# Performance work log

Hardware: AMD Instinct MI355X
Metric: run time of the kernel (lower is better)

The kernel has to match this reference:

```python
import jax, jax.numpy as jnp
import numpy as np

N = 50000      # nodes
NE = 512000    # edges
D = 128        # in_dim = out_dim
H = 8          # heads
DH = D // H    # 16, head dim
EPS_BN = 1e-5


def _bn(x, g, b):
    # training-mode BatchNorm1d: biased batch stats
    m = x.mean(0)
    v = x.var(0)
    return g * (x - m) / jnp.sqrt(v + EPS_BN) + b


def setup_inputs() -> dict:
    key = jax.random.key(0)
    ks = jax.random.split(key, 16)
    s = 0.02
    return {
        "h": jax.random.normal(ks[0], (N, D), jnp.float32),
        "e": jax.random.normal(ks[1], (NE, D), jnp.float32),
        "src": jax.random.randint(ks[2], (NE,), 0, N, jnp.int32),
        "dst": jax.random.randint(ks[3], (NE,), 0, N, jnp.int32),
        "Wq": jax.random.normal(ks[4], (D, D), jnp.float32) * s,
        "Wk": jax.random.normal(ks[5], (D, D), jnp.float32) * s,
        "Wv": jax.random.normal(ks[6], (D, D), jnp.float32) * s,
        "We": jax.random.normal(ks[7], (D, D), jnp.float32) * s,
        "Wo": jax.random.normal(ks[8], (D, D), jnp.float32) * s,
        "bo": jnp.zeros((D,), jnp.float32),
        "g1h": jnp.ones((D,), jnp.float32), "b1h": jnp.zeros((D,), jnp.float32),
        "g1e": jnp.ones((D,), jnp.float32), "b1e": jnp.zeros((D,), jnp.float32),
        "W1": jax.random.normal(ks[9], (D, 2 * D), jnp.float32) * s,
        "b1": jnp.zeros((2 * D,), jnp.float32),
        "W2": jax.random.normal(ks[10], (2 * D, D), jnp.float32) * s,
        "b2": jnp.zeros((D,), jnp.float32),
        "g2h": jnp.ones((D,), jnp.float32), "b2h": jnp.zeros((D,), jnp.float32),
    }


def reference(h, e, src, dst, Wq, Wk, Wv, We, Wo, bo,
              g1h, b1h, g1e, b1e, W1, b1, W2, b2, g2h, b2h):
    # --- multi-head edge attention ---
    Q = (h @ Wq).reshape(N, H, DH)
    K = (h @ Wk).reshape(N, H, DH)
    V = (h @ Wv).reshape(N, H, DH)
    Eh = (e @ We).reshape(NE, H, DH)
    # per-edge score: K[src]*Q[dst] / sqrt(DH), times edge features, exp-clamped
    score = (K[src] * Q[dst]) / np.sqrt(DH) * Eh            # [NE,H,DH]
    s = jnp.exp(jnp.clip(score.sum(-1), -5.0, 5.0))          # [NE,H]
    # scatter-sum to destination nodes
    wV = jax.ops.segment_sum(V[src] * s[:, :, None], dst, num_segments=N)  # [N,H,DH]
    z = jax.ops.segment_sum(s, dst, num_segments=N)                         # [N,H]
    h_attn = wV / (z[:, :, None] + 1e-6)

    # --- output proj + residual + batch norm ---
    h2 = h_attn.reshape(N, D) @ Wo + bo
    h2 = h + h2
    e2 = e + Eh.reshape(NE, D)
    h2 = _bn(h2, g1h, b1h)
    e2 = _bn(e2, g1e, b1e)

    # --- FFN + residual + batch norm ---
    r = jax.nn.relu(h2 @ W1 + b1) @ W2 + b2
    h3 = _bn(h2 + r, g2h, b2h)
    return h3, e2
```

## Files before the change

### kernel.cpp

```cpp
#include <hip/hip_runtime.h>
#include <math.h>

#define NN 50000
#define NEDGE 512000
#define DD 128

typedef short bf16x8 __attribute__((ext_vector_type(8)));
typedef float f32x4 __attribute__((ext_vector_type(4)));

__device__ __forceinline__ short f2bf(float f){
  union { float f; unsigned u; } v; v.f = f;
  unsigned u = v.u;
  return (short)((u + 0x7fffu + ((u >> 16) & 1u)) >> 16);
}
__device__ __forceinline__ float bf2f(short s){
  union { unsigned u; float f; } v; v.u = ((unsigned)(unsigned short)s) << 16; return v.f;
}

__device__ __forceinline__ bf16x8 packA(const float* __restrict__ rowp, int kbase){
  float4 x = *(const float4*)(rowp + kbase);
  float4 y = *(const float4*)(rowp + kbase + 4);
  bf16x8 r;
  r[0]=f2bf(x.x); r[1]=f2bf(x.y); r[2]=f2bf(x.z); r[3]=f2bf(x.w);
  r[4]=f2bf(y.x); r[5]=f2bf(y.y); r[6]=f2bf(y.z); r[7]=f2bf(y.w);
  return r;
}

__global__ __launch_bounds__(256) void prep_hist(
    const float* __restrict__ Wq, const float* __restrict__ Wk,
    const float* __restrict__ Wv, const float* __restrict__ We,
    const float* __restrict__ Wo, const float* __restrict__ W1,
    const float* __restrict__ W2, short* __restrict__ wdst,
    const int* __restrict__ dst, int* __restrict__ counts){
  if (blockIdx.x >= 576){
    int id = (blockIdx.x-576)*256 + threadIdx.x;
    if (id < NEDGE) atomicAdd(&counts[dst[id]], 1);
    return;
  }
  int id = blockIdx.x*256 + threadIdx.x;
  const float* src; short* dstp; int K, NCOL, local;
  if (id < 81920){
    int m = id >> 14; local = id & 16383; K = 128; NCOL = 128;
    src = (m==0)?Wq:(m==1)?Wk:(m==2)?Wv:(m==3)?We:Wo;
    dstp = wdst + m*16384;
  } else if (id < 114688){
    local = id - 81920; K = 128; NCOL = 256; src = W1; dstp = wdst + 81920;
  } else if (id < 147456){
    local = id - 114688; K = 256; NCOL = 128; src = W2; dstp = wdst + 114688;
  } else return;
  int k = local / NCOL, n = local % NCOL;
  dstp[n*K + k] = f2bf(src[local]);
}

#define SCAN_NB 196
__global__ __launch_bounds__(256) void scan_p1(
    const int* __restrict__ counts, int* __restrict__ bsum){
  int idx = blockIdx.x*256 + threadIdx.x;
  int v = (idx < NN) ? counts[idx] : 0;
  __shared__ int sd[256];
  sd[threadIdx.x] = v; __syncthreads();
  for (int o=128;o>0;o>>=1){
    if (threadIdx.x < o) sd[threadIdx.x] += sd[threadIdx.x+o];
    __syncthreads();
  }
  if (threadIdx.x == 0) bsum[blockIdx.x] = sd[0];
}
__global__ __launch_bounds__(256) void scan_p2(
    const int* __restrict__ bsum, int* __restrict__ bbase){
  int t = threadIdx.x;
  int v = (t < SCAN_NB) ? bsum[t] : 0;
  __shared__ int ps[256];
  ps[t] = v; __syncthreads();
  for (int o=1;o<256;o<<=1){
    int x = (t>=o) ? ps[t-o] : 0;
    __syncthreads();
    ps[t] += x;
    __syncthreads();
  }
  if (t < SCAN_NB) bbase[t] = ps[t] - v;
}
__global__ __launch_bounds__(256) void scan_p3(
    const int* __restrict__ counts, const int* __restrict__ bbase,
    int* __restrict__ off){
  int t = threadIdx.x;
  int idx = blockIdx.x*256 + t;
  int v = (idx < NN) ? counts[idx] : 0;
  __shared__ int ps[256];
  ps[t] = v; __syncthreads();
  for (int o=1;o<256;o<<=1){
    int x = (t>=o) ? ps[t-o] : 0;
    __syncthreads();
    ps[t] += x;
    __syncthreads();
  }
  if (idx < NN) off[idx] = bbase[blockIdx.x] + ps[t] - v;
  if (blockIdx.x == 0 && t == 0) off[NN] = NEDGE;
}

__global__ __launch_bounds__(256) void qkv_scatter(
    const float* __restrict__ h, const short* __restrict__ wT,
    short* __restrict__ QbP, short* __restrict__ KbP, short* __restrict__ Vb,
    const int* __restrict__ dst, const int* __restrict__ off,
    int* __restrict__ cursor, int* __restrict__ perm){
  if (blockIdx.x >= 782){
    int id = (blockIdx.x-782)*256 + threadIdx.x;
    if (id < NEDGE){
      int d = dst[id];
      int r = atomicAdd(&cursor[d], 1);
      perm[off[d] + r] = id;
    }
    return;
  }
  const short* WqT = wT;
  const short* WkT = wT + 16384;
  const short* WvT = wT + 32768;
  int lane = threadIdx.x & 63, wave = threadIdx.x >> 6;
  int r16 = lane & 15, kg = lane >> 4;
  int rowbase = blockIdx.x*64 + wave*16;
  int arow = rowbase + r16; if (arow > NN-1) arow = NN-1;
  const float* Arow = h + (size_t)arow*DD;
  f32x4 acc[3][8];
  #pragma unroll
  for (int m=0;m<3;m++)
    #pragma unroll
    for (int j=0;j<8;j++) acc[m][j] = (f32x4){0.f,0.f,0.f,0.f};
  #pragma unroll
  for (int kc=0;kc<4;kc++){
    int kb = kc*32 + kg*8;
    bf16x8 a = packA(Arow, kb);
    #pragma unroll
    for (int j=0;j<8;j++){
      bf16x8 bq = *(const bf16x8*)(WqT + (j*16+r16)*DD + kb);
      acc[0][j] = __builtin_amdgcn_mfma_f32_16x16x32_bf16(a, bq, acc[0][j], 0,0,0);
      bf16x8 bk = *(const bf16x8*)(WkT + (j*16+r16)*DD + kb);
      acc[1][j] = __builtin_amdgcn_mfma_f32_16x16x32_bf16(a, bk, acc[1][j], 0,0,0);
      bf16x8 bv = *(const bf16x8*)(WvT + (j*16+r16)*DD + kb);
      acc[2][j] = __builtin_amdgcn_mfma_f32_16x16x32_bf16(a, bv, acc[2][j], 0,0,0);
    }
  }
  int orow0 = rowbase + kg*4;
  #pragma unroll
  for (int j=0;j<8;j++){
    #pragma unroll
    for (int r=0;r<4;r++){
      int row = orow0 + r;
      if (row < NN){
        QbP[(size_t)row*DD + r16*8 + j] = f2bf(acc[0][j][r]);
        KbP[(size_t)row*DD + r16*8 + j] = f2bf(acc[1][j][r]);
        Vb [(size_t)row*DD + j*16 + r16] = f2bf(acc[2][j][r]);
      }
    }
  }
}

__global__ __launch_bounds__(256) void edge_fused(
    const float* __restrict__ e, const short* __restrict__ WeT,
    const short* __restrict__ QbP, const short* __restrict__ KbP,
    const int* __restrict__ src, const int* __restrict__ dst,
    short* __restrict__ e2p, short* __restrict__ sArrB,
    short* __restrict__ partB){
  __shared__ short eL[64*128];
  int tid = threadIdx.x;
  int rowbase = blockIdx.x*64;
  int lane = tid & 63, wave = tid >> 6;
  int c = lane & 15, kg = lane >> 4;
  bf16x8 kv[4], qv[4];
  #pragma unroll
  for (int r=0;r<4;r++){
    int ed = rowbase + wave*16 + kg*4 + r;
    int sj = src[ed], dj = dst[ed];
    kv[r] = *(const bf16x8*)(KbP + (size_t)sj*DD + c*8);
    qv[r] = *(const bf16x8*)(QbP + (size_t)dj*DD + c*8);
  }
  {
    int row = wave*16 + (lane >> 2);
    int c0  = (lane & 3) * 32;
    const float* rp = e + (size_t)(rowbase+row)*DD + c0;
    #pragma unroll
    for (int g=0; g<4; ++g){
      float4 x = *(const float4*)(rp + g*8);
      float4 y = *(const float4*)(rp + g*8 + 4);
      bf16x8 v;
      v[0]=f2bf(x.x); v[1]=f2bf(x.y); v[2]=f2bf(x.z); v[3]=f2bf(x.w);
      v[4]=f2bf(y.x); v[5]=f2bf(y.y); v[6]=f2bf(y.z); v[7]=f2bf(y.w);
      int col8 = (c0 >> 3) + g;
      *(bf16x8*)&eL[row*DD + ((col8 ^ (row&7))<<3)] = v;
    }
  }
  f32x4 acc[8];
  #pragma unroll
  for (int j=0;j<8;j++) acc[j] = (f32x4){0.f,0.f,0.f,0.f};
  int arow = wave*16 + c;
  #pragma unroll
  for (int kc=0;kc<4;kc++){
    int col8 = kc*4 + kg;
    bf16x8 a = *(const bf16x8*)&eL[arow*DD + ((col8 ^ (arow&7))<<3)];
    int kb = kc*32 + kg*8;
    #pragma unroll
    for (int j=0;j<8;j++){
      bf16x8 b = *(const bf16x8*)(WeT + (j*16+c)*DD + kb);
      acc[j] = __builtin_amdgcn_mfma_f32_16x16x32_bf16(a, b, acc[j], 0,0,0);
    }
  }
  float ssum[8], ssq[8];
  #pragma unroll
  for (int j=0;j<8;j++){ ssum[j]=0.f; ssq[j]=0.f; }
  #pragma unroll
  for (int r=0;r<4;r++){
    int le = wave*16 + kg*4 + r;
    int sw = le & 7;
    int rowoff = le*DD;
    #pragma unroll
    for (int j=0;j<8;j++){
      int col = j*16 + c;
      int sidx = rowoff + (((col>>3) ^ sw)<<3) + (col & 7);
      float v = bf2f(eL[sidx]) + acc[j][r];
      eL[sidx] = f2bf(v);
      ssum[j] += v; ssq[j] += v*v;
    }
  }
  #pragma unroll
  for (int j=0;j<8;j++){
    ssum[j] += __shfl_xor(ssum[j],16); ssum[j] += __shfl_xor(ssum[j],32);
    ssq[j]  += __shfl_xor(ssq[j],16);  ssq[j]  += __shfl_xor(ssq[j],32);
  }
  if (kg == 0){
    size_t pb = ((size_t)blockIdx.x*4 + wave)*256;
    #pragma unroll
    for (int j=0;j<8;j++){
      partB[pb + j*16 + c]       = f2bf(ssum[j]);
      partB[pb + 128 + j*16 + c] = f2bf(ssq[j]);
    }
  }
  #pragma unroll
  for (int r=0;r<4;r++){
    int ed = rowbase + wave*16 + kg*4 + r;
    float sreg = 0.f;
    #pragma unroll
    for (int j=0;j<8;j++){
      float p = bf2f(kv[r][j]) * bf2f(qv[r][j]) * acc[j][r];
      p += __shfl_xor(p,1); p += __shfl_xor(p,2);
      p += __shfl_xor(p,4); p += __shfl_xor(p,8);
      if (c == j) sreg = p;
    }
    if (c < 8){
      float s = __expf(fminf(fmaxf(sreg*0.25f,-5.f),5.f));
      sArrB[(size_t)ed*8 + c] = f2bf(s);
    }
  }
  #pragma unroll
  for (int it=0; it<4; ++it){
    int row = wave*16 + it*4 + (lane>>4);
    int col8 = lane & 15;
    bf16x8 v = *(const bf16x8*)&eL[row*DD + ((col8 ^ (row&7))<<3)];
    *(bf16x8*)(e2p + (size_t)(rowbase+row)*DD + col8*8) = v;
  }
}

__global__ __launch_bounds__(256) void agg_bn(
    const int* __restrict__ off, const int* __restrict__ perm,
    const int* __restrict__ src, const short* __restrict__ sArrB,
    const short* __restrict__ Vb, short* __restrict__ hA,
    const short* __restrict__ e2p, const float* __restrict__ ssE,
    float* __restrict__ e2){
  if (blockIdx.x >= 12500){
    size_t gi0 = (size_t)(blockIdx.x-12500)*256 + threadIdx.x;
    int col0 = (int)(gi0 & 15) * 8;
    float scr[8], shr[8];
    #pragma unroll
    for (int i=0;i<8;i++){ scr[i]=ssE[col0+i]; shr[i]=ssE[DD+col0+i]; }
    size_t stride = (size_t)2048*256;
    size_t total = (size_t)NEDGE*16;
    for (size_t gi = gi0; gi < total; gi += stride){
      bf16x8 v = *(const bf16x8*)(e2p + gi*8);
      float4 o0, o1;
      o0.x = bf2f(v[0])*scr[0]+shr[0];
      o0.y = bf2f(v[1])*scr[1]+shr[1];
      o0.z = bf2f(v[2])*scr[2]+shr[2];
      o0.w = bf2f(v[3])*scr[3]+shr[3];
      o1.x = bf2f(v[4])*scr[4]+shr[4];
      o1.y = bf2f(v[5])*scr[5]+shr[5];
      o1.z = bf2f(v[6])*scr[6]+shr[6];
      o1.w = bf2f(v[7])*scr[7]+shr[7];
      *(float4*)(e2 + gi*8)     = o0;
      *(float4*)(e2 + gi*8 + 4) = o1;
    }
    return;
  }
  int wave = threadIdx.x >> 6, lane = threadIdx.x & 63;
  int node = blockIdx.x*4 + wave;
  if (node >= NN) return;
  int beg = off[node], end = off[node+1];
  int col2 = lane*2;
  int hd = lane >> 3;
  float w0 = 0.f, w1 = 0.f, zh = 0.f;
  int ed = beg;
  for (; ed+3 < end; ed += 4){
    int pe0 = perm[ed],   pe1 = perm[ed+1];
    int pe2 = perm[ed+2], pe3 = perm[ed+3];
    int sj0 = src[pe0], sj1 = src[pe1], sj2 = src[pe2], sj3 = src[pe3];
    float s0 = bf2f(sArrB[(size_t)pe0*8 + hd]);
    float s1 = bf2f(sArrB[(size_t)pe1*8 + hd]);
    float s2 = bf2f(sArrB[(size_t)pe2*8 + hd]);
    float s3 = bf2f(sArrB[(size_t)pe3*8 + hd]);
    unsigned v0 = *(const unsigned*)(Vb + (size_t)sj0*DD + col2);
    unsigned v1 = *(const unsigned*)(Vb + (size_t)sj1*DD + col2);
    unsigned v2 = *(const unsigned*)(Vb + (size_t)sj2*DD + col2);
    unsigned v3 = *(const unsigned*)(Vb + (size_t)sj3*DD + col2);
    w0 += bf2f((short)(v0 & 0xffff))*s0 + bf2f((short)(v1 & 0xffff))*s1
        + bf2f((short)(v2 & 0xffff))*s2 + bf2f((short)(v3 & 0xffff))*s3;
    w1 += bf2f((short)(v0 >> 16))*s0 + bf2f((short)(v1 >> 16))*s1
        + bf2f((short)(v2 >> 16))*s2 + bf2f((short)(v3 >> 16))*s3;
    zh += s0 + s1 + s2 + s3;
  }
  for (; ed < end; ++ed){
    int pe = perm[ed];
    int sj = src[pe];
    float s = bf2f(sArrB[(size_t)pe*8 + hd]);
    unsigned vv = *(const unsigned*)(Vb + (size_t)sj*DD + col2);
    w0 += bf2f((short)(vv & 0xffff)) * s;
    w1 += bf2f((short)(vv >> 16)) * s;
    zh += s;
  }
  float inv = 1.f/(zh + 1e-6f);
  unsigned outv = (((unsigned)(unsigned short)f2bf(w1*inv)) << 16)
                |  ((unsigned)(unsigned short)f2bf(w0*inv));
  *(unsigned*)(hA + (size_t)node*DD + col2) = outv;
}

__global__ __launch_bounds__(256) void attn_out(
    const short* __restrict__ hA,
    const short* __restrict__ WoT, const float* __restrict__ bo,
    const float* __restrict__ h, short* __restrict__ h2pre,
    float* __restrict__ part){
  int lane = threadIdx.x & 63, wave = threadIdx.x >> 6;
  int r16 = lane & 15, kg = lane >> 4;
  int rowbase = blockIdx.x*64 + wave*16;
  int arow = rowbase + r16; if (arow > NN-1) arow = NN-1;
  const short* Arow = hA + (size_t)arow*DD;
  f32x4 acc[8];
  #pragma unroll
  for (int j=0;j<8;j++) acc[j] = (f32x4){0.f,0.f,0.f,0.f};
  #pragma unroll
  for (int kc=0;kc<4;kc++){
    int kb = kc*32 + kg*8;
    bf16x8 a = *(const bf16x8*)(Arow + kb);
    #pragma unroll
    for (int j=0;j<8;j++){
      bf16x8 b = *(const bf16x8*)(WoT + (j*16+r16)*DD + kb);
      acc[j] = __builtin_amdgcn_mfma_f32_16x16x32_bf16(a, b, acc[j], 0,0,0);
    }
  }
  int orow0 = rowbase + kg*4;
  float ssum[8], ssq[8];
  #pragma unroll
  for (int j=0;j<8;j++){ ssum[j]=0.f; ssq[j]=0.f; }
  #pragma unroll
  for (int j=0;j<8;j++){
    #pragma unroll
    for (int r=0;r<4;r++){
      int row = orow0 + r;
      if (row < NN){
        int col = j*16 + r16;
        float v = acc[j][r] + bo[col] + h[(size_t)row*DD + col];
        h2pre[(size_t)row*DD + col] = f2bf(v);
        ssum[j] += v; ssq[j] += v*v;
      }
    }
  }
  #pragma unroll
  for (int j=0;j<8;j++){
    ssum[j] += __shfl_xor(ssum[j],16); ssum[j] += __shfl_xor(ssum[j],32);
    ssq[j]  += __shfl_xor(ssq[j],16);  ssq[j]  += __shfl_xor(ssq[j],32);
  }
  if (kg == 0){
    size_t pb = ((size_t)blockIdx.x*4 + wave)*256;
    #pragma unroll
    for (int j=0;j<8;j++){
      part[pb + j*16 + r16]       = ssum[j];
      part[pb + 128 + j*16 + r16] = ssq[j];
    }
  }
}

__global__ __launch_bounds__(256) void ffn1_gemm(
    const short* __restrict__ h2pre, const float* __restrict__ ss1,
    const short* __restrict__ W1T, const float* __restrict__ b1,
    short* __restrict__ ffn1){
  int lane = threadIdx.x & 63, wave = threadIdx.x >> 6;
  int r16 = lane & 15, kg = lane >> 4;
  int rowbase = blockIdx.x*64 + wave*16;
  int arow = rowbase + r16; if (arow > NN-1) arow = NN-1;
  const short* Arow = h2pre + (size_t)arow*DD;
  f32x4 acc[16];
  #pragma unroll
  for (int j=0;j<16;j++) acc[j] = (f32x4){0.f,0.f,0.f,0.f};
  #pragma unroll
  for (int kc=0;kc<4;kc++){
    int kb = kc*32 + kg*8;
    bf16x8 raw = *(const bf16x8*)(Arow + kb);
    float4 s0 = *(const float4*)(ss1 + kb);
    float4 s1 = *(const float4*)(ss1 + kb + 4);
    float4 t0 = *(const float4*)(ss1 + DD + kb);
    float4 t1 = *(const float4*)(ss1 + DD + kb + 4);
    bf16x8 a;
    a[0]=f2bf(bf2f(raw[0])*s0.x+t0.x); a[1]=f2bf(bf2f(raw[1])*s0.y+t0.y);
    a[2]=f2bf(bf2f(raw[2])*s0.z+t0.z); a[3]=f2bf(bf2f(raw[3])*s0.w+t0.w);
    a[4]=f2bf(bf2f(raw[4])*s1.x+t1.x); a[5]=f2bf(bf2f(raw[5])*s1.y+t1.y);
    a[6]=f2bf(bf2f(raw[6])*s1.z+t1.z); a[7]=f2bf(bf2f(raw[7])*s1.w+t1.w);
    #pragma unroll
    for (int j=0;j<16;j++){
      bf16x8 b = *(const bf16x8*)(W1T + (j*16+r16)*DD + kb);
      acc[j] = __builtin_amdgcn_mfma_f32_16x16x32_bf16(a, b, acc[j], 0,0,0);
    }
  }
  int orow0 = rowbase + kg*4;
  #pragma unroll
  for (int j=0;j<16;j++){
    #pragma unroll
    for (int r=0;r<4;r++){
      int row = orow0 + r;
      if (row < NN){
        int col = j*16 + r16;
        float v = fmaxf(acc[j][r] + b1[col], 0.f);
        ffn1[(size_t)row*256 + col] = f2bf(v);
      }
    }
  }
}

__global__ __launch_bounds__(256) void ffn2_gemm(
    const short* __restrict__ ffn1, const short* __restrict__ W2T,
    const float* __restrict__ b2, const short* __restrict__ h2pre,
    const float* __restrict__ ss1, float* __restrict__ h3pre,
    float* __restrict__ part){
  int lane = threadIdx.x & 63, wave = threadIdx.x >> 6;
  int r16 = lane & 15, kg = lane >> 4;
  int rowbase = blockIdx.x*64 + wave*16;
  int arow = rowbase + r16; if (arow > NN-1) arow = NN-1;
  const short* Arow = ffn1 + (size_t)arow*256;
  f32x4 acc[8];
  #pragma unroll
  for (int j=0;j<8;j++) acc[j] = (f32x4){0.f,0.f,0.f,0.f};
  #pragma unroll
  for (int kc=0;kc<8;kc++){
    int kb = kc*32 + kg*8;
    bf16x8 a = *(const bf16x8*)(Arow + kb);
    #pragma unroll
    for (int j=0;j<8;j++){
      bf16x8 b = *(const bf16x8*)(W2T + (j*16+r16)*256 + kb);
      acc[j] = __builtin_amdgcn_mfma_f32_16x16x32_bf16(a, b, acc[j], 0,0,0);
    }
  }
  int orow0 = rowbase + kg*4;
  float ssum[8], ssq[8];
  #pragma unroll
  for (int j=0;j<8;j++){ ssum[j]=0.f; ssq[j]=0.f; }
  #pragma unroll
  for (int j=0;j<8;j++){
    #pragma unroll
    for (int r=0;r<4;r++){
      int row = orow0 + r;
      if (row < NN){
        int col = j*16 + r16;
        float x = bf2f(h2pre[(size_t)row*DD + col]);
        float h2bn = x*ss1[col] + ss1[DD+col];
        float v = h2bn + acc[j][r] + b2[col];
        h3pre[(size_t)row*DD + col] = v;
        ssum[j] += v; ssq[j] += v*v;
      }
    }
  }
  #pragma unroll
  for (int j=0;j<8;j++){
    ssum[j] += __shfl_xor(ssum[j],16); ssum[j] += __shfl_xor(ssum[j],32);
    ssq[j]  += __shfl_xor(ssq[j],16);  ssq[j]  += __shfl_xor(ssq[j],32);
  }
  if (kg == 0){
    size_t pb = ((size_t)blockIdx.x*4 + wave)*256;
    #pragma unroll
    for (int j=0;j<8;j++){
      part[pb + j*16 + r16]       = ssum[j];
      part[pb + 128 + j*16 + r16] = ssq[j];
    }
  }
}

__global__ __launch_bounds__(256) void bn_reduce(
    const float* __restrict__ part, int nparts, float inv_n,
    const float* __restrict__ g, const float* __restrict__ b,
    float* __restrict__ ss){
  int col = blockIdx.x, t = threadIdx.x;
  float s = 0.f, q = 0.f;
  for (int i=t; i<nparts; i+=256){
    s += part[(size_t)i*256 + col];
    q += part[(size_t)i*256 + DD + col];
  }
  __shared__ float ls[256], lq[256];
  ls[t] = s; lq[t] = q; __syncthreads();
  for (int o2=128; o2>0; o2>>=1){
    if (t < o2){ ls[t] += ls[t+o2]; lq[t] += lq[t+o2]; }
    __syncthreads();
  }
  if (t == 0){
    float mean = ls[0]*inv_n;
    float var  = lq[0]*inv_n - mean*mean;
    float sc = g[col]*rsqrtf(var + 1e-5f);
    ss[col]      = sc;
    ss[DD + col] = b[col] - mean*sc;
  }
}

__global__ __launch_bounds__(256) void bn_reduce_bf16(
    const short* __restrict__ part, int nparts, float inv_n,
    const float* __restrict__ g, const float* __restrict__ b,
    float* __restrict__ ss){
  int col = blockIdx.x, t = threadIdx.x;
  float s = 0.f, q = 0.f;
  for (int i=t; i<nparts; i+=256){
    s += bf2f(part[(size_t)i*256 + col]);
    q += bf2f(part[(size_t)i*256 + DD + col]);
  }
  __shared__ float ls[256], lq[256];
  ls[t] = s; lq[t] = q; __syncthreads();
  for (int o2=128; o2>0; o2>>=1){
    if (t < o2){ ls[t] += ls[t+o2]; lq[t] += lq[t+o2]; }
    __syncthreads();
  }
  if (t == 0){
    float mean = ls[0]*inv_n;
    float var  = lq[0]*inv_n - mean*mean;
    float sc = g[col]*rsqrtf(var + 1e-5f);
    ss[col]      = sc;
    ss[DD + col] = b[col] - mean*sc;
  }
}

__global__ __launch_bounds__(256) void bn_apply(
    float* __restrict__ x, size_t rows, const float* __restrict__ ss){
  size_t id = (size_t)blockIdx.x*256 + threadIdx.x;
  size_t total = rows*32;
  if (id >= total) return;
  float4* p = (float4*)x + id;
  int c = (int)(id & 31) * 4;
  float4 v = *p;
  v.x = v.x*ss[c]   + ss[DD+c];
  v.y = v.y*ss[c+1] + ss[DD+c+1];
  v.z = v.z*ss[c+2] + ss[DD+c+2];
  v.w = v.w*ss[c+3] + ss[DD+c+3];
  *p = v;
}

extern "C" void kernel_launch(void* const* d_in, const int* in_sizes, int n_in,
                              void* d_out, int out_size, void* d_ws, size_t ws_size,
                              hipStream_t stream){
  const float* h   = (const float*)d_in[0];
  const float* e   = (const float*)d_in[1];
  const int*   src = (const int*)d_in[2];
  const int*   dst = (const int*)d_in[3];
  const float* Wq  = (const float*)d_in[4];
  const float* Wk  = (const float*)d_in[5];
  const float* Wv  = (const float*)d_in[6];
  const float* We  = (const float*)d_in[7];
  const float* Wo  = (const float*)d_in[8];
  const float* bo  = (const float*)d_in[9];
  const float* g1h = (const float*)d_in[10];
  const float* b1h = (const float*)d_in[11];
  const float* g1e = (const float*)d_in[12];
  const float* b1e = (const float*)d_in[13];
  const float* W1  = (const float*)d_in[14];
  const float* b1  = (const float*)d_in[15];
  const float* W2  = (const float*)d_in[16];
  const float* b2  = (const float*)d_in[17];
  const float* g2h = (const float*)d_in[18];
  const float* b2h = (const float*)d_in[19];

  float* out = (float*)d_out;
  float* h3  = out;
  float* e2  = out + (size_t)NN*DD;

  char* ws = (char*)d_ws;
  size_t off_b = 0;
  auto take = [&](size_t bytes)->char*{
    char* p = ws + off_b; off_b = (off_b + bytes + 255) & ~(size_t)255; return p;
  };
  short* wT     = (short*)take((size_t)147456*2);
  float* ssE    = (float*)take(256*4);
  float* ss1    = (float*)take(256*4);
  float* ss2    = (float*)take(256*4);
  short* QbP    = (short*)take((size_t)NN*DD*2);
  short* KbP    = (short*)take((size_t)NN*DD*2);
  short* Vb     = (short*)take((size_t)NN*DD*2);
  short* hA     = (short*)take((size_t)NN*DD*2);
  short* e2p    = (short*)take((size_t)NEDGE*DD*2);
  short* sArrB  = (short*)take((size_t)NEDGE*8*2);
  int*   cnt2   = (int*)take((size_t)2*NN*4);
  int*   counts = cnt2;
  int*   cursor = cnt2 + NN;
  int*   offs   = (int*)take((size_t)(NN+1)*4);
  int*   perm   = (int*)take((size_t)NEDGE*4);
  int*   bsum   = (int*)take((size_t)256*4);
  int*   bbase  = (int*)take((size_t)256*4);
  short* h2pre  = (short*)take((size_t)NN*DD*2);
  short* ffn1   = (short*)take((size_t)NN*256*2);
  short* partEB = (short*)take((size_t)32000*256*2);
  float* partH2 = (float*)take((size_t)3128*256*4);
  float* partH3 = (float*)take((size_t)3128*256*4);

  hipMemsetAsync(cnt2, 0, (size_t)2*NN*4, stream);

  prep_hist<<<2576,256,0,stream>>>(Wq,Wk,Wv,We,Wo,W1,W2,wT, dst, counts);
  scan_p1<<<SCAN_NB,256,0,stream>>>(counts, bsum);
  scan_p2<<<1,256,0,stream>>>(bsum, bbase);
  scan_p3<<<SCAN_NB,256,0,stream>>>(counts, bbase, offs);
  qkv_scatter<<<2782,256,0,stream>>>(h, wT, QbP, KbP, Vb, dst, offs, cursor, perm);
  edge_fused<<<8000,256,0,stream>>>(e, wT+49152, QbP, KbP, src, dst,
                                    e2p, sArrB, partEB);
  bn_reduce_bf16<<<128,256,0,stream>>>(partEB, 32000, 1.f/(float)NEDGE, g1e, b1e, ssE);
  agg_bn<<<14548,256,0,stream>>>(offs, perm, src, sArrB, Vb, hA, e2p, ssE, e2);
  attn_out<<<782,256,0,stream>>>(hA, wT+65536, bo, h, h2pre, partH2);
  bn_reduce<<<128,256,0,stream>>>(partH2, 3128, 1.f/(float)NN, g1h, b1h, ss1);
  ffn1_gemm<<<782,256,0,stream>>>(h2pre, ss1, wT+81920, b1, ffn1);
  ffn2_gemm<<<782,256,0,stream>>>(ffn1, wT+114688, b2, h2pre, ss1, h3, partH3);
  bn_reduce<<<128,256,0,stream>>>(partH3, 3128, 1.f/(float)NN, g2h, b2h, ss2);
  bn_apply<<<6250,256,0,stream>>>(h3, (size_t)NN, ss2);
}
```

Measured before the change: 674.9 us.

## Scatter edge scores and sources into dst-sorted order, bf16 pre-BN h3 buffer

The scatter pass now records each edge's sorted position and writes src in dst-sorted order. The edge kernel writes attention scores directly at that sorted position, so aggregation reads srcS and sS contiguously instead of going through perm. The per-head score reduction uses a butterfly shuffle tree that needs fewer shuffles. The FFN2 pre-BN output is stored as bf16 and the final BN reads bf16 and writes fp32, which halves the intermediate traffic at the cost of extra rounding before normalization.

```diff
diff --git a/kernel.cpp b/kernel.cpp
--- a/kernel.cpp
+++ b/kernel.cpp
@@ -100,14 +100,17 @@
 __global__ __launch_bounds__(256) void qkv_scatter(
     const float* __restrict__ h, const short* __restrict__ wT,
     short* __restrict__ QbP, short* __restrict__ KbP, short* __restrict__ Vb,
-    const int* __restrict__ dst, const int* __restrict__ off,
-    int* __restrict__ cursor, int* __restrict__ perm){
+    const int* __restrict__ src, const int* __restrict__ dst,
+    const int* __restrict__ off, int* __restrict__ cursor,
+    int* __restrict__ invpos, int* __restrict__ srcS){
   if (blockIdx.x >= 782){
     int id = (blockIdx.x-782)*256 + threadIdx.x;
     if (id < NEDGE){
       int d = dst[id];
       int r = atomicAdd(&cursor[d], 1);
-      perm[off[d] + r] = id;
+      int pos = off[d] + r;
+      invpos[id] = pos;
+      srcS[pos] = src[id];
     }
     return;
   }
@@ -157,7 +160,8 @@
     const float* __restrict__ e, const short* __restrict__ WeT,
     const short* __restrict__ QbP, const short* __restrict__ KbP,
     const int* __restrict__ src, const int* __restrict__ dst,
-    short* __restrict__ e2p, short* __restrict__ sArrB,
+    const int* __restrict__ invpos,
+    short* __restrict__ e2p, short* __restrict__ sS,
     short* __restrict__ partB){
   __shared__ short eL[64*128];
   int tid = threadIdx.x;
@@ -165,10 +169,12 @@
   int lane = tid & 63, wave = tid >> 6;
   int c = lane & 15, kg = lane >> 4;
   bf16x8 kv[4], qv[4];
+  int pos_r[4];
   #pragma unroll
   for (int r=0;r<4;r++){
     int ed = rowbase + wave*16 + kg*4 + r;
     int sj = src[ed], dj = dst[ed];
+    pos_r[r] = invpos[ed];
     kv[r] = *(const bf16x8*)(KbP + (size_t)sj*DD + c*8);
     qv[r] = *(const bf16x8*)(QbP + (size_t)dj*DD + c*8);
   }
@@ -234,18 +240,25 @@
   }
   #pragma unroll
   for (int r=0;r<4;r++){
-    int ed = rowbase + wave*16 + kg*4 + r;
-    float sreg = 0.f;
-    #pragma unroll
-    for (int j=0;j<8;j++){
-      float p = bf2f(kv[r][j]) * bf2f(qv[r][j]) * acc[j][r];
-      p += __shfl_xor(p,1); p += __shfl_xor(p,2);
-      p += __shfl_xor(p,4); p += __shfl_xor(p,8);
-      if (c == j) sreg = p;
-    }
-    if (c < 8){
-      float s = __expf(fminf(fmaxf(sreg*0.25f,-5.f),5.f));
-      sArrB[(size_t)ed*8 + c] = f2bf(s);
+    float p0 = bf2f(kv[r][0])*bf2f(qv[r][0])*acc[0][r];
+    float p1 = bf2f(kv[r][1])*bf2f(qv[r][1])*acc[1][r];
+    float p2 = bf2f(kv[r][2])*bf2f(qv[r][2])*acc[2][r];
+    float p3 = bf2f(kv[r][3])*bf2f(qv[r][3])*acc[3][r];
+    float p4 = bf2f(kv[r][4])*bf2f(qv[r][4])*acc[4][r];
+    float p5 = bf2f(kv[r][5])*bf2f(qv[r][5])*acc[5][r];
+    float p6 = bf2f(kv[r][6])*bf2f(qv[r][6])*acc[6][r];
+    float p7 = bf2f(kv[r][7])*bf2f(qv[r][7])*acc[7][r];
+    float a0 = (c&8) ? (p4 + __shfl_xor(p4,8)) : (p0 + __shfl_xor(p0,8));
+    float a1 = (c&8) ? (p5 + __shfl_xor(p5,8)) : (p1 + __shfl_xor(p1,8));
+    float a2 = (c&8) ? (p6 + __shfl_xor(p6,8)) : (p2 + __shfl_xor(p2,8));
+    float a3 = (c&8) ? (p7 + __shfl_xor(p7,8)) : (p3 + __shfl_xor(p3,8));
+    float b0 = (c&4) ? (a2 + __shfl_xor(a2,4)) : (a0 + __shfl_xor(a0,4));
+    float b1 = (c&4) ? (a3 + __shfl_xor(a3,4)) : (a1 + __shfl_xor(a1,4));
+    float c0 = (c&2) ? (b1 + __shfl_xor(b1,2)) : (b0 + __shfl_xor(b0,2));
+    float u  = c0 + __shfl_xor(c0,1);
+    if (!(c & 1)){
+      float s = __expf(fminf(fmaxf(u*0.25f,-5.f),5.f));
+      sS[(size_t)pos_r[r]*8 + (c>>1)] = f2bf(s);
     }
   }
   #pragma unroll
@@ -258,9 +271,9 @@
 }
 
 __global__ __launch_bounds__(256) void agg_bn(
-    const int* __restrict__ off, const int* __restrict__ perm,
-    const int* __restrict__ src, const short* __restrict__ sArrB,
-    const short* __restrict__ Vb, short* __restrict__ hA,
+    const int* __restrict__ off, const int* __restrict__ srcS,
+    const short* __restrict__ sS, const short* __restrict__ Vb,
+    short* __restrict__ hA,
     const short* __restrict__ e2p, const float* __restrict__ ssE,
     float* __restrict__ e2){
   if (blockIdx.x >= 12500){
@@ -296,13 +309,12 @@
   float w0 = 0.f, w1 = 0.f, zh = 0.f;
   int ed = beg;
   for (; ed+3 < end; ed += 4){
-    int pe0 = perm[ed],   pe1 = perm[ed+1];
-    int pe2 = perm[ed+2], pe3 = perm[ed+3];
-    int sj0 = src[pe0], sj1 = src[pe1], sj2 = src[pe2], sj3 = src[pe3];
-    float s0 = bf2f(sArrB[(size_t)pe0*8 + hd]);
-    float s1 = bf2f(sArrB[(size_t)pe1*8 + hd]);
-    float s2 = bf2f(sArrB[(size_t)pe2*8 + hd]);
-    float s3 = bf2f(sArrB[(size_t)pe3*8 + hd]);
+    int sj0 = srcS[ed],   sj1 = srcS[ed+1];
+    int sj2 = srcS[ed+2], sj3 = srcS[ed+3];
+    float s0 = bf2f(sS[(size_t)(ed  )*8 + hd]);
+    float s1 = bf2f(sS[(size_t)(ed+1)*8 + hd]);
+    float s2 = bf2f(sS[(size_t)(ed+2)*8 + hd]);
+    float s3 = bf2f(sS[(size_t)(ed+3)*8 + hd]);
     unsigned v0 = *(const unsigned*)(Vb + (size_t)sj0*DD + col2);
     unsigned v1 = *(const unsigned*)(Vb + (size_t)sj1*DD + col2);
     unsigned v2 = *(const unsigned*)(Vb + (size_t)sj2*DD + col2);
@@ -314,9 +326,8 @@
     zh += s0 + s1 + s2 + s3;
   }
   for (; ed < end; ++ed){
-    int pe = perm[ed];
-    int sj = src[pe];
-    float s = bf2f(sArrB[(size_t)pe*8 + hd]);
+    int sj = srcS[ed];
+    float s = bf2f(sS[(size_t)ed*8 + hd]);
     unsigned vv = *(const unsigned*)(Vb + (size_t)sj*DD + col2);
     w0 += bf2f((short)(vv & 0xffff)) * s;
     w1 += bf2f((short)(vv >> 16)) * s;
@@ -432,7 +443,7 @@
 __global__ __launch_bounds__(256) void ffn2_gemm(
     const short* __restrict__ ffn1, const short* __restrict__ W2T,
     const float* __restrict__ b2, const short* __restrict__ h2pre,
-    const float* __restrict__ ss1, float* __restrict__ h3pre,
+    const float* __restrict__ ss1, short* __restrict__ h3p,
     float* __restrict__ part){
   int lane = threadIdx.x & 63, wave = threadIdx.x >> 6;
   int r16 = lane & 15, kg = lane >> 4;
@@ -466,7 +477,7 @@
         float x = bf2f(h2pre[(size_t)row*DD + col]);
         float h2bn = x*ss1[col] + ss1[DD+col];
         float v = h2bn + acc[j][r] + b2[col];
-        h3pre[(size_t)row*DD + col] = v;
+        h3p[(size_t)row*DD + col] = f2bf(v);
         ssum[j] += v; ssq[j] += v*v;
       }
     }
@@ -536,19 +547,24 @@
   }
 }
 
-__global__ __launch_bounds__(256) void bn_apply(
-    float* __restrict__ x, size_t rows, const float* __restrict__ ss){
-  size_t id = (size_t)blockIdx.x*256 + threadIdx.x;
-  size_t total = rows*32;
-  if (id >= total) return;
-  float4* p = (float4*)x + id;
-  int c = (int)(id & 31) * 4;
-  float4 v = *p;
-  v.x = v.x*ss[c]   + ss[DD+c];
-  v.y = v.y*ss[c+1] + ss[DD+c+1];
-  v.z = v.z*ss[c+2] + ss[DD+c+2];
-  v.w = v.w*ss[c+3] + ss[DD+c+3];
-  *p = v;
+__global__ __launch_bounds__(256) void bn_apply_h(
+    const short* __restrict__ h3p, const float* __restrict__ ss,
+    float* __restrict__ h3){
+  size_t gi = (size_t)blockIdx.x*256 + threadIdx.x;
+  if (gi >= (size_t)NN*16) return;
+  int col0 = (int)(gi & 15) * 8;
+  bf16x8 v = *(const bf16x8*)(h3p + gi*8);
+  float4 o0, o1;
+  o0.x = bf2f(v[0])*ss[col0+0]+ss[DD+col0+0];
+  o0.y = bf2f(v[1])*ss[col0+1]+ss[DD+col0+1];
+  o0.z = bf2f(v[2])*ss[col0+2]+ss[DD+col0+2];
+  o0.w = bf2f(v[3])*ss[col0+3]+ss[DD+col0+3];
+  o1.x = bf2f(v[4])*ss[col0+4]+ss[DD+col0+4];
+  o1.y = bf2f(v[5])*ss[col0+5]+ss[DD+col0+5];
+  o1.z = bf2f(v[6])*ss[col0+6]+ss[DD+col0+6];
+  o1.w = bf2f(v[7])*ss[col0+7]+ss[DD+col0+7];
+  *(float4*)(h3 + gi*8)     = o0;
+  *(float4*)(h3 + gi*8 + 4) = o1;
 }
 
 extern "C" void kernel_launch(void* const* d_in, const int* in_sizes, int n_in,
@@ -593,16 +609,18 @@
   short* Vb     = (short*)take((size_t)NN*DD*2);
   short* hA     = (short*)take((size_t)NN*DD*2);
   short* e2p    = (short*)take((size_t)NEDGE*DD*2);
-  short* sArrB  = (short*)take((size_t)NEDGE*8*2);
+  short* sS     = (short*)take((size_t)NEDGE*8*2);
   int*   cnt2   = (int*)take((size_t)2*NN*4);
   int*   counts = cnt2;
   int*   cursor = cnt2 + NN;
   int*   offs   = (int*)take((size_t)(NN+1)*4);
-  int*   perm   = (int*)take((size_t)NEDGE*4);
+  int*   invpos = (int*)take((size_t)NEDGE*4);
+  int*   srcS   = (int*)take((size_t)NEDGE*4);
   int*   bsum   = (int*)take((size_t)256*4);
   int*   bbase  = (int*)take((size_t)256*4);
   short* h2pre  = (short*)take((size_t)NN*DD*2);
   short* ffn1   = (short*)take((size_t)NN*256*2);
+  short* h3p    = (short*)take((size_t)NN*DD*2);
   short* partEB = (short*)take((size_t)32000*256*2);
   float* partH2 = (float*)take((size_t)3128*256*4);
   float* partH3 = (float*)take((size_t)3128*256*4);
@@ -613,15 +631,16 @@
   scan_p1<<<SCAN_NB,256,0,stream>>>(counts, bsum);
   scan_p2<<<1,256,0,stream>>>(bsum, bbase);
   scan_p3<<<SCAN_NB,256,0,stream>>>(counts, bbase, offs);
-  qkv_scatter<<<2782,256,0,stream>>>(h, wT, QbP, KbP, Vb, dst, offs, cursor, perm);
-  edge_fused<<<8000,256,0,stream>>>(e, wT+49152, QbP, KbP, src, dst,
-                                    e2p, sArrB, partEB);
+  qkv_scatter<<<2782,256,0,stream>>>(h, wT, QbP, KbP, Vb, src, dst, offs,
+                                     cursor, invpos, srcS);
+  edge_fused<<<8000,256,0,stream>>>(e, wT+49152, QbP, KbP, src, dst, invpos,
+                                    e2p, sS, partEB);
   bn_reduce_bf16<<<128,256,0,stream>>>(partEB, 32000, 1.f/(float)NEDGE, g1e, b1e, ssE);
-  agg_bn<<<14548,256,0,stream>>>(offs, perm, src, sArrB, Vb, hA, e2p, ssE, e2);
+  agg_bn<<<14548,256,0,stream>>>(offs, srcS, sS, Vb, hA, e2p, ssE, e2);
   attn_out<<<782,256,0,stream>>>(hA, wT+65536, bo, h, h2pre, partH2);
   bn_reduce<<<128,256,0,stream>>>(partH2, 3128, 1.f/(float)NN, g1h, b1h, ss1);
   ffn1_gemm<<<782,256,0,stream>>>(h2pre, ss1, wT+81920, b1, ffn1);
-  ffn2_gemm<<<782,256,0,stream>>>(ffn1, wT+114688, b2, h2pre, ss1, h3, partH3);
+  ffn2_gemm<<<782,256,0,stream>>>(ffn1, wT+114688, b2, h2pre, ss1, h3p, partH3);
   bn_reduce<<<128,256,0,stream>>>(partH3, 3128, 1.f/(float)NN, g2h, b2h, ss2);
-  bn_apply<<<6250,256,0,stream>>>(h3, (size_t)NN, ss2);
-}
+  bn_apply_h<<<3125,256,0,stream>>>(h3p, ss2, h3);
+}
```

Result: no change. 668.0 us, median of 2 (-1.0%).
